# Kernel optimization log

Hardware: AMD Instinct MI355X
Metric: run time of the kernel (lower is better)

## Reference

```python
import jax, jax.numpy as jnp
import numpy as np

NUM_FREQS = 6

def posenc(x, num_freqs):
    freqs = (2.0 ** jnp.arange(num_freqs)).astype(x.dtype)  # [F]
    ang = x[..., None] * freqs                               # [N, D, F]
    enc = jnp.concatenate([jnp.sin(ang), jnp.cos(ang)], axis=-1)  # [N, D, 2F]
    return enc.reshape(x.shape[0], -1)

def setup_inputs() -> dict:
    key = jax.random.key(0)
    k1, k2, k3 = jax.random.split(key, 3)
    N, D, C = 200000, 6, 256
    E = D * 2 * NUM_FREQS  # 72
    X = jax.random.normal(k1, (N, D), dtype=jnp.float32)
    linear_mappings = jax.random.normal(k2, (3 * C, E), dtype=jnp.float32) * 0.05
    centroids = jax.random.normal(k3, (C, 3), dtype=jnp.float32)
    return {"X": X, "linear_mappings": linear_mappings, "centroids": centroids}

def reference(X, linear_mappings, centroids):
    N = X.shape[0]
    encoded_X = posenc(X, NUM_FREQS)                         # [N, E]
    rgb_clusters = encoded_X @ linear_mappings.T             # [N, 3C]
    rgb_clusters = rgb_clusters.reshape(N, -1, 3)            # [N, C, 3]
    # scores = centroids @ X[:, :3].T  -> softmax over clusters per point
    scores = X[:, :3] @ centroids.T                          # [N, C] (== scores.T in torch code)
    attention_weights = jax.nn.softmax(scores, axis=-1)      # [N, C]
    # torch does diagonal(attn @ rgb_clusters).T == per-row contraction:
    rgb = jnp.einsum('nc,ncd->nd', attention_weights, rgb_clusters)  # [N, 3]
    return rgb
```

## Files before the change

kernel.cpp:

```cpp
#include <hip/hip_runtime.h>
#include <math.h>


#define NCLUST   256
#define M_BLK    32
#define THREADS  64
#define NTILES   15
#define BG_BYTES (NTILES * 8 * 64 * 16)
#define ET_STRIDE 72

typedef __attribute__((ext_vector_type(8))) short bfrag_t;
typedef __attribute__((ext_vector_type(4))) float cfrag_t;
typedef __attribute__((ext_vector_type(4))) unsigned int uifrag_t;

static __device__ __forceinline__ unsigned short f2bf1(float f) {
    return __builtin_bit_cast(unsigned short, (__bf16)f);
}
static __device__ __forceinline__ unsigned int f2bf2(float lo, float hi) {
    return (unsigned int)f2bf1(lo) | ((unsigned int)f2bf1(hi) << 16);
}
static __device__ __forceinline__ float bf2f(unsigned short s) {
    return __uint_as_float(((unsigned int)s) << 16);
}

__global__ void prep_kernel(const float* __restrict__ W, uint4* __restrict__ Bg) {
    const int u = blockIdx.x * 256 + threadIdx.x;
    if (u >= NTILES * 8 * 64) return;
    const int lane = u & 63, ks = (u >> 6) & 7, tile = u >> 9;
    const int ln = lane & 15, q = lane >> 4;
    const int jp = tile * 16 + ln;
    const int d  = jp / 80;
    const int e  = jp - d * 80;
    const int c0 = ks * 32 + q * 8;
    unsigned int w[4] = {0u, 0u, 0u, 0u};
    if (e < 72) {
#pragma unroll
        for (int i = 0; i < 4; ++i) {
            float f0 = W[((c0 + 2 * i)     * 3 + d) * 72 + e];
            float f1 = W[((c0 + 2 * i + 1) * 3 + d) * 72 + e];
            w[i] = f2bf2(f0, f1);
        }
    }
    Bg[u] = make_uint4(w[0], w[1], w[2], w[3]);
}

__global__ __launch_bounds__(THREADS, 2) void rgb_attn_mfma(
    const float* __restrict__ X,
    const float* __restrict__ cent,
    const void* __restrict__ Bg,
    float* __restrict__ out, int N)
{
    __shared__ __align__(16) float Xs[M_BLK * 6];
    __shared__ __align__(16) unsigned char encT[80 * ET_STRIDE];

    const int lane = threadIdx.x;
    const int q    = lane >> 4;
    const int ln   = lane & 15;
    const int mbase = blockIdx.x * M_BLK;

    if (mbase + M_BLK <= N) {
        if (lane < 48) {
            const float4 v = *(const float4*)(X + (size_t)mbase * 6 + lane * 4);
            *(float4*)(Xs + lane * 4) = v;
        }
    } else {
#pragma unroll 1
        for (int i = lane; i < M_BLK * 6; i += 64) {
            const int p  = mbase + i / 6;
            const int pc = (p < N) ? p : (N - 1);
            Xs[i] = X[pc * 6 + (i % 6)];
        }
    }

    const char* Bgc = (const char*)Bg + lane * 16;
    bfrag_t bcur[8], bnext[8];
#pragma unroll
    for (int ks = 0; ks < 8; ++ks)
        bcur[ks] = *(const bfrag_t*)(Bgc + ks * 1024);

    {
        const int pt = lane & 31;
        const int h  = lane >> 5;
        unsigned char* colp = encT + pt * 2;
#pragma unroll
        for (int k = 0; k < 3; ++k) {
            const int dd = 3 * h + k;
            const float xv = Xs[pt * 6 + dd];
            float s[6], c[6];
            __sincosf(xv, &s[0], &c[0]);
#pragma unroll
            for (int f = 1; f < 6; ++f) {
                s[f] = 2.0f * s[f-1] * c[f-1];
                c[f] = 1.0f - 2.0f * s[f-1] * s[f-1];
            }
#pragma unroll
            for (int f = 0; f < 6; ++f) {
                *(unsigned short*)(colp + (dd*12 + f)     * ET_STRIDE) = f2bf1(s[f]);
                *(unsigned short*)(colp + (dd*12 + 6 + f) * ET_STRIDE) = f2bf1(c[f]);
            }
        }
        *(uint2*)(encT + (72 + (lane >> 3)) * ET_STRIDE + (lane & 7) * 8) = make_uint2(0u, 0u);
    }

    uifrag_t afrag[2][8];
    float dA = 0.0f, dB = 0.0f;
    {
        const float x00 = Xs[ln * 6 + 0], x01 = Xs[ln * 6 + 1], x02 = Xs[ln * 6 + 2];
        const float x10 = Xs[(16 + ln) * 6 + 0], x11 = Xs[(16 + ln) * 6 + 1],
                    x12 = Xs[(16 + ln) * 6 + 2];
        const float4* c4base = (const float4*)cent;
#pragma unroll
        for (int g = 0; g < 8; ++g) {
            const float4* c4 = c4base + (6 * q + 24 * g);
            const float4 v0 = c4[0], v1 = c4[1], v2 = c4[2];
            const float4 v3 = c4[3], v4 = c4[4], v5 = c4[5];
            float cx[8], cy[8], cz[8];
            cx[0]=v0.x; cy[0]=v0.y; cz[0]=v0.z;
            cx[1]=v0.w; cy[1]=v1.x; cz[1]=v1.y;
            cx[2]=v1.z; cy[2]=v1.w; cz[2]=v2.x;
            cx[3]=v2.y; cy[3]=v2.z; cz[3]=v2.w;
            cx[4]=v3.x; cy[4]=v3.y; cz[4]=v3.z;
            cx[5]=v3.w; cy[5]=v4.x; cz[5]=v4.y;
            cx[6]=v4.z; cy[6]=v4.w; cz[6]=v5.x;
            cx[7]=v5.y; cy[7]=v5.z; cz[7]=v5.w;
            float ea[8], eb[8];
#pragma unroll
            for (int j = 0; j < 8; ++j) {
                ea[j] = __expf(fmaf(x00, cx[j], fmaf(x01, cy[j], x02 * cz[j])));
                eb[j] = __expf(fmaf(x10, cx[j], fmaf(x11, cy[j], x12 * cz[j])));
                dA += ea[j]; dB += eb[j];
            }
#pragma unroll
            for (int w = 0; w < 4; ++w) {
                afrag[0][g][w] = f2bf2(ea[2*w], ea[2*w+1]);
                afrag[1][g][w] = f2bf2(eb[2*w], eb[2*w+1]);
            }
        }
    }

    float part[3][2][4] = {};
#pragma unroll
    for (int d = 0; d < 3; ++d) {
#pragma unroll 1
        for (int tt = 0; tt < 5; ++tt) {
            const int t = d * 5 + tt;
            if (t < NTILES - 1) {
#pragma unroll
                for (int ks = 0; ks < 8; ++ks)
                    bnext[ks] = *(const bfrag_t*)(Bgc + (t + 1) * 8192 + ks * 1024);
            }
            cfrag_t a0 = {0.f,0.f,0.f,0.f}, a1 = {0.f,0.f,0.f,0.f};
#pragma unroll
            for (int ks = 0; ks < 8; ++ks) {
                a0 = __builtin_amdgcn_mfma_f32_16x16x32_bf16(
                         __builtin_bit_cast(bfrag_t, afrag[0][ks]), bcur[ks], a0, 0, 0, 0);
                a1 = __builtin_amdgcn_mfma_f32_16x16x32_bf16(
                         __builtin_bit_cast(bfrag_t, afrag[1][ks]), bcur[ks], a1, 0, 0, 0);
            }
            const unsigned char* ep = encT + (tt * 16 + ln) * ET_STRIDE + q * 8;
#pragma unroll
            for (int mt = 0; mt < 2; ++mt) {
                const ushort4 ev = *(const ushort4*)(ep + mt * 32);
                const cfrag_t a = mt ? a1 : a0;
                part[d][mt][0] = fmaf(a[0], bf2f(ev.x), part[d][mt][0]);
                part[d][mt][1] = fmaf(a[1], bf2f(ev.y), part[d][mt][1]);
                part[d][mt][2] = fmaf(a[2], bf2f(ev.z), part[d][mt][2]);
                part[d][mt][3] = fmaf(a[3], bf2f(ev.w), part[d][mt][3]);
            }
#pragma unroll
            for (int ks = 0; ks < 8; ++ks)
                bcur[ks] = bnext[ks];
        }
    }

#pragma unroll
    for (int mask = 1; mask <= 8; mask <<= 1)
#pragma unroll
        for (int d = 0; d < 3; ++d)
#pragma unroll
            for (int mt = 0; mt < 2; ++mt)
#pragma unroll
                for (int r = 0; r < 4; ++r)
                    part[d][mt][r] += __shfl_xor(part[d][mt][r], mask, 64);

    dA += __shfl_xor(dA, 16, 64); dA += __shfl_xor(dA, 32, 64);
    dB += __shfl_xor(dB, 16, 64); dB += __shfl_xor(dB, 32, 64);
    const float iA = 1.0f / dA;
    const float iB = 1.0f / dB;
    float invr[2][4];
#pragma unroll
    for (int r = 0; r < 4; ++r) {
        invr[0][r] = __shfl(iA, q * 4 + r, 64);
        invr[1][r] = __shfl(iB, q * 4 + r, 64);
    }

    if (ln == 0) {
#pragma unroll
        for (int mt = 0; mt < 2; ++mt)
#pragma unroll
            for (int r = 0; r < 4; ++r) {
                const int pm = mt * 16 + q * 4 + r;
                const int g  = mbase + pm;
                if (g < N) {
                    out[g*3+0] = part[0][mt][r] * invr[mt][r];
                    out[g*3+1] = part[1][mt][r] * invr[mt][r];
                    out[g*3+2] = part[2][mt][r] * invr[mt][r];
                }
            }
    }
}

__global__ __launch_bounds__(256) void rgb_attn_fallback(
    const float* __restrict__ X, const float* __restrict__ W,
    const float* __restrict__ cent, float* __restrict__ out, int N)
{
    const int n = blockIdx.x * 256 + threadIdx.x;
    const bool valid = (n < N);
    float x[6];
#pragma unroll
    for (int k = 0; k < 6; ++k) x[k] = valid ? X[n * 6 + k] : 0.0f;
    float enc[72];
#pragma unroll
    for (int d = 0; d < 6; ++d)
#pragma unroll
        for (int f = 0; f < 6; ++f) {
            float s, c;
            __sincosf(x[d] * (float)(1 << f), &s, &c);
            enc[d*12+f] = s; enc[d*12+6+f] = c;
        }
    float acc0 = 0, acc1 = 0, acc2 = 0, denom = 0;
#pragma unroll 1
    for (int c = 0; c < NCLUST; ++c) {
        float s = fmaf(x[0], cent[c*3], fmaf(x[1], cent[c*3+1], x[2]*cent[c*3+2]));
        float ew = __expf(s);
        const float* w = W + c * 216;
        float d0 = 0, d1 = 0, d2 = 0;
#pragma unroll
        for (int e = 0; e < 72; ++e) {
            float ee = enc[e];
            d0 = fmaf(ee, w[e], d0);
            d1 = fmaf(ee, w[72 + e], d1);
            d2 = fmaf(ee, w[144 + e], d2);
        }
        denom += ew;
        acc0 = fmaf(ew, d0, acc0); acc1 = fmaf(ew, d1, acc1); acc2 = fmaf(ew, d2, acc2);
    }
    if (valid) {
        float inv = 1.0f / denom;
        out[n*3+0] = acc0*inv; out[n*3+1] = acc1*inv; out[n*3+2] = acc2*inv;
    }
}

extern "C" void kernel_launch(void* const* d_in, const int* in_sizes, int n_in,
                              void* d_out, int out_size, void* d_ws, size_t ws_size,
                              hipStream_t stream)
{
    const float* X    = (const float*)d_in[0];
    const float* W    = (const float*)d_in[1];
    const float* cent = (const float*)d_in[2];
    float* out = (float*)d_out;
    const int N = in_sizes[0] / 6;

    if (ws_size >= (size_t)BG_BYTES) {
        uint4* Bg = (uint4*)d_ws;
        prep_kernel<<<(NTILES * 8 * 64 + 255) / 256, 256, 0, stream>>>(W, Bg);
        const int blocks = (N + M_BLK - 1) / M_BLK;
        rgb_attn_mfma<<<blocks, THREADS, 0, stream>>>(X, cent, (const void*)Bg, out, N);
    } else {
        rgb_attn_fallback<<<(N + 255) / 256, 256, 0, stream>>>(X, W, cent, out, N);
    }
}
```

Measured before the change: 122.0 us.

## Stream weight tiles through an LDS double buffer via direct global-to-LDS loads

Replaces the register double buffer of B fragments (bcur/bnext, 16 vector registers of 8 shorts) with two 8 KB LDS buffers. These are filled by `global_load_lds` 16-byte direct loads, prefetching the next tile while the current one is consumed. Each tile's fragments are read from LDS in two halves of four just before the MFMAs. The aim is to cut VGPR pressure and register copies, improving occupancy and latency hiding. The cost is 16 KB more LDS per block, an explicit `vmcnt(0)` wait each tile, and extra LDS read traffic.

Measured after the change: 111.4 us. 8.7% less time.

```diff
diff --git a/kernel.cpp b/kernel.cpp
--- a/kernel.cpp
+++ b/kernel.cpp
@@ -21,6 +21,11 @@
 }
 static __device__ __forceinline__ float bf2f(unsigned short s) {
     return __uint_as_float(((unsigned int)s) << 16);
+}
+static __device__ __forceinline__ void glds16(const void* g, void* l) {
+    __builtin_amdgcn_global_load_lds(
+        (const __attribute__((address_space(1))) unsigned int*)g,
+        (__attribute__((address_space(3))) unsigned int*)l, 16, 0, 0);
 }
 
 __global__ void prep_kernel(const float* __restrict__ W, uint4* __restrict__ Bg) {
@@ -52,6 +57,7 @@
 {
     __shared__ __align__(16) float Xs[M_BLK * 6];
     __shared__ __align__(16) unsigned char encT[80 * ET_STRIDE];
+    __shared__ __align__(16) unsigned char Bb[2][8192];
 
     const int lane = threadIdx.x;
     const int q    = lane >> 4;
@@ -72,11 +78,9 @@
         }
     }
 
-    const char* Bgc = (const char*)Bg + lane * 16;
-    bfrag_t bcur[8], bnext[8];
-#pragma unroll
-    for (int ks = 0; ks < 8; ++ks)
-        bcur[ks] = *(const bfrag_t*)(Bgc + ks * 1024);
+#pragma unroll
+    for (int i = 0; i < 8; ++i)
+        glds16((const char*)Bg + (i * 64 + lane) * 16, (char*)Bb[0] + i * 1024);
 
     {
         const int pt = lane & 31;
@@ -144,32 +148,74 @@
 #pragma unroll 1
         for (int tt = 0; tt < 5; ++tt) {
             const int t = d * 5 + tt;
+            const unsigned char* bb = Bb[t & 1];
+
+            asm volatile("s_waitcnt vmcnt(0)" ::: "memory");
+            __builtin_amdgcn_sched_barrier(0);
+
+            bfrag_t b0 = *(const bfrag_t*)(bb + (0 * 64 + lane) * 16);
+            bfrag_t b1 = *(const bfrag_t*)(bb + (1 * 64 + lane) * 16);
+            bfrag_t b2 = *(const bfrag_t*)(bb + (2 * 64 + lane) * 16);
+            bfrag_t b3 = *(const bfrag_t*)(bb + (3 * 64 + lane) * 16);
+            const unsigned char* ep = encT + (tt * 16 + ln) * ET_STRIDE + q * 8;
+            const ushort4 ev0 = *(const ushort4*)(ep);
+            const ushort4 ev1 = *(const ushort4*)(ep + 32);
+
             if (t < NTILES - 1) {
-#pragma unroll
-                for (int ks = 0; ks < 8; ++ks)
-                    bnext[ks] = *(const bfrag_t*)(Bgc + (t + 1) * 8192 + ks * 1024);
-            }
+                const char* gsrc = (const char*)Bg + (t + 1) * 8192;
+                char* ldst = (char*)Bb[(t + 1) & 1];
+#pragma unroll
+                for (int i = 0; i < 8; ++i)
+                    glds16(gsrc + (i * 64 + lane) * 16, ldst + i * 1024);
+            }
+
             cfrag_t a0 = {0.f,0.f,0.f,0.f}, a1 = {0.f,0.f,0.f,0.f};
-#pragma unroll
-            for (int ks = 0; ks < 8; ++ks) {
-                a0 = __builtin_amdgcn_mfma_f32_16x16x32_bf16(
-                         __builtin_bit_cast(bfrag_t, afrag[0][ks]), bcur[ks], a0, 0, 0, 0);
-                a1 = __builtin_amdgcn_mfma_f32_16x16x32_bf16(
-                         __builtin_bit_cast(bfrag_t, afrag[1][ks]), bcur[ks], a1, 0, 0, 0);
-            }
-            const unsigned char* ep = encT + (tt * 16 + ln) * ET_STRIDE + q * 8;
-#pragma unroll
-            for (int mt = 0; mt < 2; ++mt) {
-                const ushort4 ev = *(const ushort4*)(ep + mt * 32);
-                const cfrag_t a = mt ? a1 : a0;
-                part[d][mt][0] = fmaf(a[0], bf2f(ev.x), part[d][mt][0]);
-                part[d][mt][1] = fmaf(a[1], bf2f(ev.y), part[d][mt][1]);
-                part[d][mt][2] = fmaf(a[2], bf2f(ev.z), part[d][mt][2]);
-                part[d][mt][3] = fmaf(a[3], bf2f(ev.w), part[d][mt][3]);
-            }
-#pragma unroll
-            for (int ks = 0; ks < 8; ++ks)
-                bcur[ks] = bnext[ks];
+            a0 = __builtin_amdgcn_mfma_f32_16x16x32_bf16(
+                     __builtin_bit_cast(bfrag_t, afrag[0][0]), b0, a0, 0, 0, 0);
+            a1 = __builtin_amdgcn_mfma_f32_16x16x32_bf16(
+                     __builtin_bit_cast(bfrag_t, afrag[1][0]), b0, a1, 0, 0, 0);
+            a0 = __builtin_amdgcn_mfma_f32_16x16x32_bf16(
+                     __builtin_bit_cast(bfrag_t, afrag[0][1]), b1, a0, 0, 0, 0);
+            a1 = __builtin_amdgcn_mfma_f32_16x16x32_bf16(
+                     __builtin_bit_cast(bfrag_t, afrag[1][1]), b1, a1, 0, 0, 0);
+            a0 = __builtin_amdgcn_mfma_f32_16x16x32_bf16(
+                     __builtin_bit_cast(bfrag_t, afrag[0][2]), b2, a0, 0, 0, 0);
+            a1 = __builtin_amdgcn_mfma_f32_16x16x32_bf16(
+                     __builtin_bit_cast(bfrag_t, afrag[1][2]), b2, a1, 0, 0, 0);
+            a0 = __builtin_amdgcn_mfma_f32_16x16x32_bf16(
+                     __builtin_bit_cast(bfrag_t, afrag[0][3]), b3, a0, 0, 0, 0);
+            a1 = __builtin_amdgcn_mfma_f32_16x16x32_bf16(
+                     __builtin_bit_cast(bfrag_t, afrag[1][3]), b3, a1, 0, 0, 0);
+
+            b0 = *(const bfrag_t*)(bb + (4 * 64 + lane) * 16);
+            b1 = *(const bfrag_t*)(bb + (5 * 64 + lane) * 16);
+            b2 = *(const bfrag_t*)(bb + (6 * 64 + lane) * 16);
+            b3 = *(const bfrag_t*)(bb + (7 * 64 + lane) * 16);
+            a0 = __builtin_amdgcn_mfma_f32_16x16x32_bf16(
+                     __builtin_bit_cast(bfrag_t, afrag[0][4]), b0, a0, 0, 0, 0);
+            a1 = __builtin_amdgcn_mfma_f32_16x16x32_bf16(
+                     __builtin_bit_cast(bfrag_t, afrag[1][4]), b0, a1, 0, 0, 0);
+            a0 = __builtin_amdgcn_mfma_f32_16x16x32_bf16(
+                     __builtin_bit_cast(bfrag_t, afrag[0][5]), b1, a0, 0, 0, 0);
+            a1 = __builtin_amdgcn_mfma_f32_16x16x32_bf16(
+                     __builtin_bit_cast(bfrag_t, afrag[1][5]), b1, a1, 0, 0, 0);
+            a0 = __builtin_amdgcn_mfma_f32_16x16x32_bf16(
+                     __builtin_bit_cast(bfrag_t, afrag[0][6]), b2, a0, 0, 0, 0);
+            a1 = __builtin_amdgcn_mfma_f32_16x16x32_bf16(
+                     __builtin_bit_cast(bfrag_t, afrag[1][6]), b2, a1, 0, 0, 0);
+            a0 = __builtin_amdgcn_mfma_f32_16x16x32_bf16(
+                     __builtin_bit_cast(bfrag_t, afrag[0][7]), b3, a0, 0, 0, 0);
+            a1 = __builtin_amdgcn_mfma_f32_16x16x32_bf16(
+                     __builtin_bit_cast(bfrag_t, afrag[1][7]), b3, a1, 0, 0, 0);
+
+            part[d][0][0] = fmaf(a0[0], bf2f(ev0.x), part[d][0][0]);
+            part[d][0][1] = fmaf(a0[1], bf2f(ev0.y), part[d][0][1]);
+            part[d][0][2] = fmaf(a0[2], bf2f(ev0.z), part[d][0][2]);
+            part[d][0][3] = fmaf(a0[3], bf2f(ev0.w), part[d][0][3]);
+            part[d][1][0] = fmaf(a1[0], bf2f(ev1.x), part[d][1][0]);
+            part[d][1][1] = fmaf(a1[1], bf2f(ev1.y), part[d][1][1]);
+            part[d][1][2] = fmaf(a1[2], bf2f(ev1.z), part[d][1][2]);
+            part[d][1][3] = fmaf(a1[3], bf2f(ev1.w), part[d][1][3]);
         }
     }
 
```
